# Performance work log

Measured on AMD Instinct MI355X. Metric: run time of the kernel, lower is better.

The kernel has to match this reference:

```python
import jax, jax.numpy as jnp
import numpy as np

N_NODES = 100000
N_EDGES = 1600000
N_GRAPHS = 256
IN_DIM, HID, OUT_DIM = 20, 128, 30954


def setup_inputs() -> dict:
    key = jax.random.key(0)
    ks = jax.random.split(key, 9)
    x = jax.random.normal(ks[0], (N_NODES, IN_DIM), dtype=jnp.float32)
    edge_index = jax.random.randint(ks[1], (2, N_EDGES), 0, N_NODES, dtype=jnp.int64)
    batch = jnp.sort(jax.random.randint(ks[2], (N_NODES,), 0, N_GRAPHS, dtype=jnp.int64))
    s = 0.05
    W1 = jax.random.normal(ks[3], (IN_DIM, HID), dtype=jnp.float32) * s
    b1 = jax.random.normal(ks[4], (HID,), dtype=jnp.float32) * s
    W2 = jax.random.normal(ks[5], (HID, HID), dtype=jnp.float32) * s
    b2 = jax.random.normal(ks[6], (HID,), dtype=jnp.float32) * s
    Wc = jax.random.normal(ks[7], (HID, OUT_DIM), dtype=jnp.float32) * s
    bc = jax.random.normal(ks[8], (OUT_DIM,), dtype=jnp.float32) * s
    return {"x": x, "edge_index": edge_index, "batch": batch,
            "W1": W1, "b1": b1, "W2": W2, "b2": b2, "Wc": Wc, "bc": bc}


def _gcn_norm(edge_index, n_nodes):
    # add self loops (PyG GCNConv default), symmetric normalization
    loops = jnp.arange(n_nodes, dtype=edge_index.dtype)
    src = jnp.concatenate([edge_index[0], loops])
    dst = jnp.concatenate([edge_index[1], loops])
    deg = jax.ops.segment_sum(jnp.ones_like(dst, dtype=jnp.float32), dst,
                              num_segments=n_nodes)
    dinv = jnp.where(deg > 0, jax.lax.rsqrt(deg), 0.0)
    norm = dinv[src] * dinv[dst]  # [E+N]
    return src, dst, norm


def _gcn_conv(x, src, dst, norm, W, b, n_nodes):
    h = x @ W                              # [N, out] transform first (fewer msg flops)
    msg = h[src] * norm[:, None]           # gather + scale
    out = jax.ops.segment_sum(msg, dst, num_segments=n_nodes)
    return out + b


def reference(x, edge_index, batch, W1, b1, W2, b2, Wc, bc):
    n = x.shape[0]
    src, dst, norm = _gcn_norm(edge_index, n)
    h = jax.nn.relu(_gcn_conv(x, src, dst, norm, W1, b1, n))
    # dropout is identity in eval mode
    h = jax.nn.relu(_gcn_conv(h, src, dst, norm, W2, b2, n))
    # global mean pool per graph
    sums = jax.ops.segment_sum(h, batch, num_segments=N_GRAPHS)       # [G, HID]
    cnts = jax.ops.segment_sum(jnp.ones((n,), jnp.float32), batch,
                               num_segments=N_GRAPHS)
    pooled = sums / jnp.maximum(cnts, 1.0)[:, None]
    return pooled @ Wc + bc  # [G, OUT_DIM]
```

## Files before the change

kernel.cpp:

```cpp
#include <hip/hip_runtime.h>

#define HID 128
#define SCAN_B 256

__device__ __forceinline__ float bf_lo(unsigned int u) { return __uint_as_float(u << 16); }
__device__ __forceinline__ float bf_hi(unsigned int u) { return __uint_as_float(u & 0xFFFF0000u); }
__device__ __forceinline__ unsigned short f2bf(float f) {
    unsigned int u = __float_as_uint(f);
    unsigned int r = (u + 0x7FFFu + ((u >> 16) & 1u)) >> 16;
    return (unsigned short)r;
}

__global__ void init_kernel(const unsigned int* __restrict__ p, int* __restrict__ flag,
                            float4* __restrict__ deg4, long long n4) {
    if (blockIdx.x == 0 && threadIdx.x == 0) {
        int is64 = 1;
        for (int i = 0; i < 64; ++i) {
            if (p[2 * i + 1] != 0u) { is64 = 0; break; }
        }
        *flag = is64;
    }
    long long i = (long long)blockIdx.x * blockDim.x + threadIdx.x;
    long long stride = (long long)gridDim.x * blockDim.x;
    for (; i < n4; i += stride) deg4[i] = make_float4(0.f, 0.f, 0.f, 0.f);
}

__global__ void cvtdeg_kernel(const void* __restrict__ p, int* __restrict__ out,
                              int* __restrict__ deg, int E, const int* __restrict__ flag) {
    int i = blockIdx.x * blockDim.x + threadIdx.x;
    if (i < 2 * E) {
        int v = (*flag) ? (int)((const long long*)p)[i] : ((const int*)p)[i];
        out[i] = v;
        if (i >= E) atomicAdd(&deg[v], 1);
    }
}

__global__ void cvtx_kernel(const float* __restrict__ x, unsigned short* __restrict__ xb, int n) {
    int i = blockIdx.x * blockDim.x + threadIdx.x;
    if (i < n) xb[i] = f2bf(x[i]);
}

__global__ __launch_bounds__(SCAN_B) void scan1_kernel(const int* __restrict__ deg,
                                                       int* __restrict__ incl,
                                                       int* __restrict__ blockSums, int N) {
    __shared__ int s[SCAN_B];
    int i = blockIdx.x * SCAN_B + threadIdx.x;
    int v = (i < N) ? deg[i] : 0;
    s[threadIdx.x] = v;
    __syncthreads();
#pragma unroll
    for (int off = 1; off < SCAN_B; off <<= 1) {
        int t = (threadIdx.x >= off) ? s[threadIdx.x - off] : 0;
        __syncthreads();
        s[threadIdx.x] += t;
        __syncthreads();
    }
    if (i < N) incl[i] = s[threadIdx.x];
    if (threadIdx.x == SCAN_B - 1) blockSums[blockIdx.x] = s[SCAN_B - 1];
}

__global__ __launch_bounds__(1024) void scan2_kernel(int* __restrict__ blockSums, int nb) {
    __shared__ int s[1024];
    int v = (threadIdx.x < nb) ? blockSums[threadIdx.x] : 0;
    s[threadIdx.x] = v;
    __syncthreads();
#pragma unroll
    for (int off = 1; off < 1024; off <<= 1) {
        int t = (threadIdx.x >= off) ? s[threadIdx.x - off] : 0;
        __syncthreads();
        s[threadIdx.x] += t;
        __syncthreads();
    }
    if (threadIdx.x < nb) blockSums[threadIdx.x] = (threadIdx.x > 0) ? s[threadIdx.x - 1] : 0;
}

__global__ void scan3_kernel(const int* __restrict__ incl, const int* __restrict__ deg,
                             const int* __restrict__ blockSums, int* __restrict__ rowstart,
                             float* __restrict__ dinv, int* __restrict__ cursor,
                             const void* __restrict__ bt, const int* __restrict__ flag,
                             int* __restrict__ gstart, int G,
                             int N, int E) {
    int i = blockIdx.x * blockDim.x + threadIdx.x;
    if (i < N) {
        int d = deg[i];
        rowstart[i] = incl[i] - d + blockSums[i / SCAN_B];
        dinv[i] = rsqrtf((float)(d + 1));
        cursor[i] = 0;
    }
    if (i == 0) rowstart[N] = E;
    if (i <= G) {
        int is64 = *flag;
        int lo = 0, hi = N;
        while (lo < hi) {
            int mid = (lo + hi) >> 1;
            int v = is64 ? (int)((const long long*)bt)[mid] : ((const int*)bt)[mid];
            if (v < i) lo = mid + 1; else hi = mid;
        }
        gstart[i] = lo;
    }
}

__global__ void scatter_kernel(const int* __restrict__ src, const int* __restrict__ dst,
                               const int* __restrict__ rowstart, int* __restrict__ cursor,
                               int2* __restrict__ elist, const float* __restrict__ dinv, int E) {
    int e = blockIdx.x * blockDim.x + threadIdx.x;
    if (e >= E) return;
    int s = src[e], d = dst[e];
    int pos = rowstart[d] + atomicAdd(&cursor[d], 1);
    float nm = dinv[s] * dinv[d];
    elist[pos] = make_int2(s, __float_as_int(nm));
}

__global__ __launch_bounds__(256) void agg_lin1_kernel(const float* __restrict__ x,
                                                       const unsigned int* __restrict__ xb32,
                                                       const float* __restrict__ W,
                                                       const float* __restrict__ b,
                                                       unsigned int* __restrict__ h1b,
                                                       const int* __restrict__ rowstart,
                                                       const int2* __restrict__ elist,
                                                       const float* __restrict__ dinv,
                                                       int N, int IN) {
    __shared__ float Ws[20 * HID];
    __shared__ float zs[8][20];
    const int tid = threadIdx.x;
    for (int i = tid; i < IN * HID; i += 256) Ws[i] = W[i];

    const int g      = tid >> 5;
    const int lane32 = tid & 31;
    const int slot   = lane32 >> 4;
    const int l      = lane32 & 15;
    const int node   = blockIdx.x * 8 + g;
    const int half   = IN >> 1;
    const bool act   = (node < N) && (l < half);

    float accx = 0.f, accy = 0.f;
    if (node < N) {
        int beg = rowstart[node], end = rowstart[node + 1];
        int e = beg + slot;
        for (; e + 6 < end; e += 8) {
            int2 p0 = elist[e];
            int2 p1 = elist[e + 2];
            int2 p2 = elist[e + 4];
            int2 p3 = elist[e + 6];
            unsigned int u0 = act ? xb32[(size_t)p0.x * half + l] : 0u;
            unsigned int u1 = act ? xb32[(size_t)p1.x * half + l] : 0u;
            unsigned int u2 = act ? xb32[(size_t)p2.x * half + l] : 0u;
            unsigned int u3 = act ? xb32[(size_t)p3.x * half + l] : 0u;
            float n0 = __int_as_float(p0.y), n1 = __int_as_float(p1.y);
            float n2 = __int_as_float(p2.y), n3 = __int_as_float(p3.y);
            accx += bf_lo(u0) * n0 + bf_lo(u1) * n1 + bf_lo(u2) * n2 + bf_lo(u3) * n3;
            accy += bf_hi(u0) * n0 + bf_hi(u1) * n1 + bf_hi(u2) * n2 + bf_hi(u3) * n3;
        }
        for (; e < end; e += 2) {
            int2 p0 = elist[e];
            unsigned int u0 = act ? xb32[(size_t)p0.x * half + l] : 0u;
            float n0 = __int_as_float(p0.y);
            accx += bf_lo(u0) * n0;
            accy += bf_hi(u0) * n0;
        }
    }
    accx += __shfl_xor(accx, 16, 64);
    accy += __shfl_xor(accy, 16, 64);
    if (node < N && slot == 0 && l < half) {
        float di = dinv[node];
        float dd = di * di;
        zs[g][2 * l]     = accx + x[(size_t)node * IN + 2 * l] * dd;
        zs[g][2 * l + 1] = accy + x[(size_t)node * IN + 2 * l + 1] * dd;
    }
    __syncthreads();

    if (node < N) {
        const int j = lane32;
        float4 acc4 = ((const float4*)b)[j];
        for (int k = 0; k < IN; ++k) {
            float zv = zs[g][k];
            float4 w = *(const float4*)&Ws[k * HID + j * 4];
            acc4.x += zv * w.x; acc4.y += zv * w.y;
            acc4.z += zv * w.z; acc4.w += zv * w.w;
        }
        acc4.x = fmaxf(acc4.x, 0.f); acc4.y = fmaxf(acc4.y, 0.f);
        acc4.z = fmaxf(acc4.z, 0.f); acc4.w = fmaxf(acc4.w, 0.f);
        uint2 st;
        st.x = (unsigned)f2bf(acc4.x) | ((unsigned)f2bf(acc4.y) << 16);
        st.y = (unsigned)f2bf(acc4.z) | ((unsigned)f2bf(acc4.w) << 16);
        ((uint2*)h1b)[(size_t)node * 32 + j] = st;
    }
}

#define TBM 64
#define TBN 64
#define TBK 32
#define XLD (TBM + 4)

__global__ __launch_bounds__(256) void gemm128_kernel(const unsigned int* __restrict__ Ab,
                                                      const float* __restrict__ W,
                                                      unsigned short* __restrict__ Cb, int N) {
    __shared__ float xs[TBK][XLD];
    __shared__ float wsh[TBK][TBN + 4];
    const int tid = threadIdx.x;
    const int n0 = blockIdx.x * TBM;
    const int c0 = blockIdx.y * TBN;
    const int ng = tid >> 4;
    const int cg = tid & 15;
    const int anode = tid >> 2;
    const int af    = tid & 3;
    const int wk    = tid >> 4;
    const int wc    = tid & 15;

    const uint4* Av = (const uint4*)Ab;

    float acc[4][4] = {};

    for (int k0 = 0; k0 < HID; k0 += TBK) {
        {
            int gn = n0 + anode;
            uint4 u = make_uint4(0u, 0u, 0u, 0u);
            if (gn < N) u = Av[(size_t)gn * 16 + (k0 >> 3) + af];
            int kb = af * 8;
            xs[kb + 0][anode] = bf_lo(u.x);
            xs[kb + 1][anode] = bf_hi(u.x);
            xs[kb + 2][anode] = bf_lo(u.y);
            xs[kb + 3][anode] = bf_hi(u.y);
            xs[kb + 4][anode] = bf_lo(u.z);
            xs[kb + 5][anode] = bf_hi(u.z);
            xs[kb + 6][anode] = bf_lo(u.w);
            xs[kb + 7][anode] = bf_hi(u.w);
        }
#pragma unroll
        for (int r = 0; r < 2; ++r) {
            int kk = wk + r * 16;
            *(float4*)&wsh[kk][wc * 4] =
                *(const float4*)(W + (size_t)(k0 + kk) * HID + c0 + wc * 4);
        }
        __syncthreads();
#pragma unroll
        for (int kk = 0; kk < TBK; ++kk) {
            float a[4], b[4];
            *(float4*)a = *(const float4*)&xs[kk][ng * 4];
            *(float4*)b = *(const float4*)&wsh[kk][cg * 4];
#pragma unroll
            for (int m = 0; m < 4; ++m)
#pragma unroll
                for (int n = 0; n < 4; ++n) acc[m][n] += a[m] * b[n];
        }
        __syncthreads();
    }

#pragma unroll
    for (int m = 0; m < 4; ++m) {
        int gn = n0 + ng * 4 + m;
        if (gn < N) {
            ushort4 st;
            st.x = f2bf(acc[m][0]); st.y = f2bf(acc[m][1]);
            st.z = f2bf(acc[m][2]); st.w = f2bf(acc[m][3]);
            *(ushort4*)(Cb + (size_t)gn * HID + c0 + cg * 4) = st;
        }
    }
}

__global__ __launch_bounds__(256) void csr_aggb_kernel(const unsigned short* __restrict__ h2b,
                                                       unsigned short* __restrict__ outb,
                                                       const int* __restrict__ rowstart,
                                                       const int2* __restrict__ elist,
                                                       const float* __restrict__ dinv,
                                                       const float* __restrict__ bias,
                                                       int N) {
    int node = blockIdx.x * 16 + (threadIdx.x >> 4);
    if (node >= N) return;
    int q = threadIdx.x & 15;
    const uint4* hv = (const uint4*)h2b;
    float acc[8] = {};
    int beg = rowstart[node], end = rowstart[node + 1];
    int e = beg;
    for (; e + 3 < end; e += 4) {
        int2 p0 = elist[e];
        int2 p1 = elist[e + 1];
        int2 p2 = elist[e + 2];
        int2 p3 = elist[e + 3];
        uint4 a0 = hv[(size_t)p0.x * 16 + q];
        uint4 a1 = hv[(size_t)p1.x * 16 + q];
        uint4 a2 = hv[(size_t)p2.x * 16 + q];
        uint4 a3 = hv[(size_t)p3.x * 16 + q];
        float n0 = __int_as_float(p0.y), n1 = __int_as_float(p1.y);
        float n2 = __int_as_float(p2.y), n3 = __int_as_float(p3.y);
        acc[0] += bf_lo(a0.x) * n0 + bf_lo(a1.x) * n1 + bf_lo(a2.x) * n2 + bf_lo(a3.x) * n3;
        acc[1] += bf_hi(a0.x) * n0 + bf_hi(a1.x) * n1 + bf_hi(a2.x) * n2 + bf_hi(a3.x) * n3;
        acc[2] += bf_lo(a0.y) * n0 + bf_lo(a1.y) * n1 + bf_lo(a2.y) * n2 + bf_lo(a3.y) * n3;
        acc[3] += bf_hi(a0.y) * n0 + bf_hi(a1.y) * n1 + bf_hi(a2.y) * n2 + bf_hi(a3.y) * n3;
        acc[4] += bf_lo(a0.z) * n0 + bf_lo(a1.z) * n1 + bf_lo(a2.z) * n2 + bf_lo(a3.z) * n3;
        acc[5] += bf_hi(a0.z) * n0 + bf_hi(a1.z) * n1 + bf_hi(a2.z) * n2 + bf_hi(a3.z) * n3;
        acc[6] += bf_lo(a0.w) * n0 + bf_lo(a1.w) * n1 + bf_lo(a2.w) * n2 + bf_lo(a3.w) * n3;
        acc[7] += bf_hi(a0.w) * n0 + bf_hi(a1.w) * n1 + bf_hi(a2.w) * n2 + bf_hi(a3.w) * n3;
    }
    for (; e < end; ++e) {
        int2 p0 = elist[e];
        uint4 a0 = hv[(size_t)p0.x * 16 + q];
        float n0 = __int_as_float(p0.y);
        acc[0] += bf_lo(a0.x) * n0; acc[1] += bf_hi(a0.x) * n0;
        acc[2] += bf_lo(a0.y) * n0; acc[3] += bf_hi(a0.y) * n0;
        acc[4] += bf_lo(a0.z) * n0; acc[5] += bf_hi(a0.z) * n0;
        acc[6] += bf_lo(a0.w) * n0; acc[7] += bf_hi(a0.w) * n0;
    }
    float di = dinv[node];
    float dd = di * di;
    uint4 sv = hv[(size_t)node * 16 + q];
    float self[8] = { bf_lo(sv.x), bf_hi(sv.x), bf_lo(sv.y), bf_hi(sv.y),
                      bf_lo(sv.z), bf_hi(sv.z), bf_lo(sv.w), bf_hi(sv.w) };
    float4 b0 = ((const float4*)bias)[2 * q];
    float4 b1 = ((const float4*)bias)[2 * q + 1];
    float r[8];
    r[0] = fmaxf(acc[0] + self[0] * dd + b0.x, 0.f);
    r[1] = fmaxf(acc[1] + self[1] * dd + b0.y, 0.f);
    r[2] = fmaxf(acc[2] + self[2] * dd + b0.z, 0.f);
    r[3] = fmaxf(acc[3] + self[3] * dd + b0.w, 0.f);
    r[4] = fmaxf(acc[4] + self[4] * dd + b1.x, 0.f);
    r[5] = fmaxf(acc[5] + self[5] * dd + b1.y, 0.f);
    r[6] = fmaxf(acc[6] + self[6] * dd + b1.z, 0.f);
    r[7] = fmaxf(acc[7] + self[7] * dd + b1.w, 0.f);
    uint4 st;
    st.x = (unsigned)f2bf(r[0]) | ((unsigned)f2bf(r[1]) << 16);
    st.y = (unsigned)f2bf(r[2]) | ((unsigned)f2bf(r[3]) << 16);
    st.z = (unsigned)f2bf(r[4]) | ((unsigned)f2bf(r[5]) << 16);
    st.w = (unsigned)f2bf(r[6]) | ((unsigned)f2bf(r[7]) << 16);
    ((uint4*)outb)[(size_t)node * 16 + q] = st;
}

__global__ __launch_bounds__(1024) void pool2_kernel(const unsigned short* __restrict__ hb,
                                                     const int* __restrict__ gstart,
                                                     float* __restrict__ meanp, int G) {
    int g = blockIdx.x;
    int part = threadIdx.x >> 7;
    int j = threadIdx.x & 127;
    int beg = gstart[g], end = gstart[g + 1];
    float s = 0.f;
    for (int n = beg + part; n < end; n += 8)
        s += __uint_as_float(((unsigned)hb[(size_t)n * HID + j]) << 16);
    __shared__ float red[8][HID];
    red[part][j] = s;
    __syncthreads();
    if (part == 0) {
        float tot = 0.f;
#pragma unroll
        for (int r = 0; r < 8; ++r) tot += red[r][j];
        float c = (float)(end - beg);
        meanp[(size_t)g * HID + j] = tot / fmaxf(c, 1.f);
    }
}

#define CBM 64
#define CBN 64
#define CBK 32

__global__ __launch_bounds__(256) void clsgemm_kernel(const float* __restrict__ A,
                                                      const float* __restrict__ Bw,
                                                      const float* __restrict__ bc,
                                                      float* __restrict__ C,
                                                      int G, int OUT) {
    __shared__ float as[CBK][CBM + 4];
    __shared__ float bs[CBK][CBN + 4];
    const int tid = threadIdx.x;
    const int g0 = blockIdx.y * CBM;
    const int c0 = blockIdx.x * CBN;
    const int mg = tid >> 4;
    const int cg = tid & 15;
    const int arow = tid >> 3;
    const int af   = tid & 7;
    const int wk   = tid >> 4;
    const int wc   = tid & 15;

    float acc[4][4] = {};

    for (int k0 = 0; k0 < HID; k0 += CBK) {
#pragma unroll
        for (int r = 0; r < 2; ++r) {
            int row = arow + r * 32;
            int g = g0 + row;
            float4 v = make_float4(0.f, 0.f, 0.f, 0.f);
            if (g < G) v = *(const float4*)(A + (size_t)g * HID + k0 + af * 4);
            as[af * 4 + 0][row] = v.x;
            as[af * 4 + 1][row] = v.y;
            as[af * 4 + 2][row] = v.z;
            as[af * 4 + 3][row] = v.w;
        }
#pragma unroll
        for (int r = 0; r < 2; ++r) {
            int kk = wk + r * 16;
            int c = c0 + wc * 4;
            const float* bp = Bw + (size_t)(k0 + kk) * OUT + c;
            float2 lo = make_float2(0.f, 0.f), hi = make_float2(0.f, 0.f);
            if (c + 3 < OUT) {
                lo = *(const float2*)bp;
                hi = *(const float2*)(bp + 2);
            } else {
                if (c + 0 < OUT) lo.x = bp[0];
                if (c + 1 < OUT) lo.y = bp[1];
                if (c + 2 < OUT) hi.x = bp[2];
                if (c + 3 < OUT) hi.y = bp[3];
            }
            bs[kk][wc * 4 + 0] = lo.x;
            bs[kk][wc * 4 + 1] = lo.y;
            bs[kk][wc * 4 + 2] = hi.x;
            bs[kk][wc * 4 + 3] = hi.y;
        }
        __syncthreads();
#pragma unroll
        for (int kk = 0; kk < CBK; ++kk) {
            float a[4], b[4];
            *(float4*)a = *(const float4*)&as[kk][mg * 4];
            *(float4*)b = *(const float4*)&bs[kk][cg * 4];
#pragma unroll
            for (int m = 0; m < 4; ++m)
#pragma unroll
                for (int n = 0; n < 4; ++n) acc[m][n] += a[m] * b[n];
        }
        __syncthreads();
    }

    int c = c0 + cg * 4;
    float b0 = (c + 0 < OUT) ? bc[c + 0] : 0.f;
    float b1 = (c + 1 < OUT) ? bc[c + 1] : 0.f;
    float b2 = (c + 2 < OUT) ? bc[c + 2] : 0.f;
    float b3 = (c + 3 < OUT) ? bc[c + 3] : 0.f;
#pragma unroll
    for (int m = 0; m < 4; ++m) {
        int g = g0 + mg * 4 + m;
        if (g >= G) continue;
        float* cp = C + (size_t)g * OUT + c;
        if (c + 3 < OUT) {
            *(float2*)cp = make_float2(acc[m][0] + b0, acc[m][1] + b1);
            *(float2*)(cp + 2) = make_float2(acc[m][2] + b2, acc[m][3] + b3);
        } else {
            if (c + 0 < OUT) cp[0] = acc[m][0] + b0;
            if (c + 1 < OUT) cp[1] = acc[m][1] + b1;
            if (c + 2 < OUT) cp[2] = acc[m][2] + b2;
            if (c + 3 < OUT) cp[3] = acc[m][3] + b3;
        }
    }
}

extern "C" void kernel_launch(void* const* d_in, const int* in_sizes, int n_in,
                              void* d_out, int out_size, void* d_ws, size_t ws_size,
                              hipStream_t stream) {
    const float* x  = (const float*)d_in[0];
    const void*  ei = d_in[1];
    const void*  bt = d_in[2];
    const float* W1 = (const float*)d_in[3];
    const float* b1 = (const float*)d_in[4];
    const float* W2 = (const float*)d_in[5];
    const float* b2 = (const float*)d_in[6];
    const float* Wc = (const float*)d_in[7];
    const float* bc = (const float*)d_in[8];
    float* out = (float*)d_out;

    const int N   = in_sizes[2];
    const int E   = in_sizes[1] / 2;
    const int IN  = in_sizes[0] / N;
    const int OUT = in_sizes[8];
    const int G   = out_size / OUT;

    char* ws = (char*)d_ws;
    size_t off = 0;
    auto alloc = [&](size_t bytes) {
        size_t p = off;
        off += (bytes + 255) & ~(size_t)255;
        return p;
    };
    int*            idx32    = (int*)(ws + alloc((size_t)2 * E * 4));
    int*            deg      = (int*)(ws + alloc((size_t)N * 4));
    float*          dinv     = (float*)(ws + alloc((size_t)N * 4));
    int*            incl     = (int*)(ws + alloc((size_t)N * 4));
    int*            rowstart = (int*)(ws + alloc((size_t)(N + 1) * 4));
    int*            cursor   = (int*)(ws + alloc((size_t)N * 4));
    int*            blockSums= (int*)(ws + alloc((size_t)1024 * 4));
    int2*           elist    = (int2*)(ws + alloc((size_t)E * 8));
    unsigned short* xb       = (unsigned short*)(ws + alloc((size_t)N * IN * 2));
    unsigned int*   h1b      = (unsigned int*)(ws + alloc((size_t)N * HID * 2));
    unsigned short* h2b      = (unsigned short*)(ws + alloc((size_t)N * HID * 2));
    unsigned short* houtb    = (unsigned short*)(ws + alloc((size_t)N * HID * 2));
    int*            gstart   = (int*)(ws + alloc((size_t)(G + 1) * 4));
    float*          meanp    = (float*)(ws + alloc((size_t)G * HID * 4));
    int*            flag     = (int*)(ws + alloc(4));
    (void)ws_size;

    int* srcI = idx32;
    int* dstI = idx32 + E;

    const int B = 256;
    const int nb = (N + SCAN_B - 1) / SCAN_B;

    init_kernel<<<256, B, 0, stream>>>((const unsigned int*)ei, flag, (float4*)deg,
                                       (long long)N / 4);
    cvtdeg_kernel<<<(2 * E + B - 1) / B, B, 0, stream>>>(ei, idx32, deg, E, flag);
    cvtx_kernel<<<(N * IN + B - 1) / B, B, 0, stream>>>(x, xb, N * IN);

    scan1_kernel<<<nb, SCAN_B, 0, stream>>>(deg, incl, blockSums, N);
    scan2_kernel<<<1, 1024, 0, stream>>>(blockSums, nb);
    scan3_kernel<<<(N + B - 1) / B, B, 0, stream>>>(incl, deg, blockSums, rowstart,
                                                    dinv, cursor, bt, flag, gstart, G, N, E);
    scatter_kernel<<<(E + B - 1) / B, B, 0, stream>>>(srcI, dstI, rowstart, cursor, elist, dinv, E);

    agg_lin1_kernel<<<(N + 7) / 8, 256, 0, stream>>>(x, (const unsigned int*)xb, W1, b1,
                                                     h1b, rowstart, elist, dinv, N, IN);

    {
        dim3 grid((N + TBM - 1) / TBM, HID / TBN);
        gemm128_kernel<<<grid, 256, 0, stream>>>(h1b, W2, h2b, N);
    }
    csr_aggb_kernel<<<(N + 15) / 16, 256, 0, stream>>>(h2b, houtb, rowstart, elist, dinv, b2, N);

    pool2_kernel<<<G, 1024, 0, stream>>>(houtb, gstart, meanp, G);

    {
        dim3 grid((OUT + CBN - 1) / CBN, (G + CBM - 1) / CBM);
        clsgemm_kernel<<<grid, 256, 0, stream>>>(meanp, Wc, bc, out, G, OUT);
    }
}
```

Measured before the change: 373.4 us.

## Factor symmetric GCN normalization into per-node scaling, shrink edge list to indices

Splits the edge weight dinv[s]*dinv[d] into a source-side scale, applied once per node when x is converted to bf16 and in the layer-2 GEMM epilogue, and a destination-side scale applied after aggregation. The edge list now stores only source indices (4 bytes instead of 8), which halves edge-list traffic in both aggregation passes and removes per-edge multiplies and the dinv gathers in scatter. The x conversion now runs after dinv is computed, and rounding to bf16 happens after pre-scaling, which slightly changes numerics.

Result: slower. 391.3 us (+4.8%).

```diff
diff --git a/kernel.cpp b/kernel.cpp
--- a/kernel.cpp
+++ b/kernel.cpp
@@ -35,9 +35,13 @@
     }
 }
 
-__global__ void cvtx_kernel(const float* __restrict__ x, unsigned short* __restrict__ xb, int n) {
+__global__ void cvtx_kernel(const float* __restrict__ x, const float* __restrict__ dinv,
+                            unsigned short* __restrict__ xb, int n, int IN) {
     int i = blockIdx.x * blockDim.x + threadIdx.x;
-    if (i < n) xb[i] = f2bf(x[i]);
+    if (i < n) {
+        int node = i / IN;
+        xb[i] = f2bf(x[i] * dinv[node]);
+    }
 }
 
 __global__ __launch_bounds__(SCAN_B) void scan1_kernel(const int* __restrict__ deg,
@@ -102,22 +106,20 @@
 
 __global__ void scatter_kernel(const int* __restrict__ src, const int* __restrict__ dst,
                                const int* __restrict__ rowstart, int* __restrict__ cursor,
-                               int2* __restrict__ elist, const float* __restrict__ dinv, int E) {
+                               int* __restrict__ elist, int E) {
     int e = blockIdx.x * blockDim.x + threadIdx.x;
     if (e >= E) return;
     int s = src[e], d = dst[e];
     int pos = rowstart[d] + atomicAdd(&cursor[d], 1);
-    float nm = dinv[s] * dinv[d];
-    elist[pos] = make_int2(s, __float_as_int(nm));
-}
-
-__global__ __launch_bounds__(256) void agg_lin1_kernel(const float* __restrict__ x,
-                                                       const unsigned int* __restrict__ xb32,
+    elist[pos] = s;
+}
+
+__global__ __launch_bounds__(256) void agg_lin1_kernel(const unsigned int* __restrict__ xb32,
                                                        const float* __restrict__ W,
                                                        const float* __restrict__ b,
                                                        unsigned int* __restrict__ h1b,
                                                        const int* __restrict__ rowstart,
-                                                       const int2* __restrict__ elist,
+                                                       const int* __restrict__ elist,
                                                        const float* __restrict__ dinv,
                                                        int N, int IN) {
     __shared__ float Ws[20 * HID];
@@ -138,34 +140,31 @@
         int beg = rowstart[node], end = rowstart[node + 1];
         int e = beg + slot;
         for (; e + 6 < end; e += 8) {
-            int2 p0 = elist[e];
-            int2 p1 = elist[e + 2];
-            int2 p2 = elist[e + 4];
-            int2 p3 = elist[e + 6];
-            unsigned int u0 = act ? xb32[(size_t)p0.x * half + l] : 0u;
-            unsigned int u1 = act ? xb32[(size_t)p1.x * half + l] : 0u;
-            unsigned int u2 = act ? xb32[(size_t)p2.x * half + l] : 0u;
-            unsigned int u3 = act ? xb32[(size_t)p3.x * half + l] : 0u;
-            float n0 = __int_as_float(p0.y), n1 = __int_as_float(p1.y);
-            float n2 = __int_as_float(p2.y), n3 = __int_as_float(p3.y);
-            accx += bf_lo(u0) * n0 + bf_lo(u1) * n1 + bf_lo(u2) * n2 + bf_lo(u3) * n3;
-            accy += bf_hi(u0) * n0 + bf_hi(u1) * n1 + bf_hi(u2) * n2 + bf_hi(u3) * n3;
+            int s0 = elist[e];
+            int s1 = elist[e + 2];
+            int s2 = elist[e + 4];
+            int s3 = elist[e + 6];
+            unsigned int u0 = act ? xb32[(size_t)s0 * half + l] : 0u;
+            unsigned int u1 = act ? xb32[(size_t)s1 * half + l] : 0u;
+            unsigned int u2 = act ? xb32[(size_t)s2 * half + l] : 0u;
+            unsigned int u3 = act ? xb32[(size_t)s3 * half + l] : 0u;
+            accx += bf_lo(u0) + bf_lo(u1) + bf_lo(u2) + bf_lo(u3);
+            accy += bf_hi(u0) + bf_hi(u1) + bf_hi(u2) + bf_hi(u3);
         }
         for (; e < end; e += 2) {
-            int2 p0 = elist[e];
-            unsigned int u0 = act ? xb32[(size_t)p0.x * half + l] : 0u;
-            float n0 = __int_as_float(p0.y);
-            accx += bf_lo(u0) * n0;
-            accy += bf_hi(u0) * n0;
+            int s0 = elist[e];
+            unsigned int u0 = act ? xb32[(size_t)s0 * half + l] : 0u;
+            accx += bf_lo(u0);
+            accy += bf_hi(u0);
         }
     }
     accx += __shfl_xor(accx, 16, 64);
     accy += __shfl_xor(accy, 16, 64);
     if (node < N && slot == 0 && l < half) {
         float di = dinv[node];
-        float dd = di * di;
-        zs[g][2 * l]     = accx + x[(size_t)node * IN + 2 * l] * dd;
-        zs[g][2 * l + 1] = accy + x[(size_t)node * IN + 2 * l + 1] * dd;
+        unsigned int us = xb32[(size_t)node * half + l];
+        zs[g][2 * l]     = di * (accx + bf_lo(us));
+        zs[g][2 * l + 1] = di * (accy + bf_hi(us));
     }
     __syncthreads();
 
@@ -194,6 +193,7 @@
 
 __global__ __launch_bounds__(256) void gemm128_kernel(const unsigned int* __restrict__ Ab,
                                                       const float* __restrict__ W,
+                                                      const float* __restrict__ dinv,
                                                       unsigned short* __restrict__ Cb, int N) {
     __shared__ float xs[TBK][XLD];
     __shared__ float wsh[TBK][TBN + 4];
@@ -250,9 +250,10 @@
     for (int m = 0; m < 4; ++m) {
         int gn = n0 + ng * 4 + m;
         if (gn < N) {
+            float di = dinv[gn];
             ushort4 st;
-            st.x = f2bf(acc[m][0]); st.y = f2bf(acc[m][1]);
-            st.z = f2bf(acc[m][2]); st.w = f2bf(acc[m][3]);
+            st.x = f2bf(acc[m][0] * di); st.y = f2bf(acc[m][1] * di);
+            st.z = f2bf(acc[m][2] * di); st.w = f2bf(acc[m][3] * di);
             *(ushort4*)(Cb + (size_t)gn * HID + c0 + cg * 4) = st;
         }
     }
@@ -261,7 +262,7 @@
 __global__ __launch_bounds__(256) void csr_aggb_kernel(const unsigned short* __restrict__ h2b,
                                                        unsigned short* __restrict__ outb,
                                                        const int* __restrict__ rowstart,
-                                                       const int2* __restrict__ elist,
+                                                       const int* __restrict__ elist,
                                                        const float* __restrict__ dinv,
                                                        const float* __restrict__ bias,
                                                        int N) {
@@ -273,50 +274,46 @@
     int beg = rowstart[node], end = rowstart[node + 1];
     int e = beg;
     for (; e + 3 < end; e += 4) {
-        int2 p0 = elist[e];
-        int2 p1 = elist[e + 1];
-        int2 p2 = elist[e + 2];
-        int2 p3 = elist[e + 3];
-        uint4 a0 = hv[(size_t)p0.x * 16 + q];
-        uint4 a1 = hv[(size_t)p1.x * 16 + q];
-        uint4 a2 = hv[(size_t)p2.x * 16 + q];
-        uint4 a3 = hv[(size_t)p3.x * 16 + q];
-        float n0 = __int_as_float(p0.y), n1 = __int_as_float(p1.y);
-        float n2 = __int_as_float(p2.y), n3 = __int_as_float(p3.y);
-        acc[0] += bf_lo(a0.x) * n0 + bf_lo(a1.x) * n1 + bf_lo(a2.x) * n2 + bf_lo(a3.x) * n3;
-        acc[1] += bf_hi(a0.x) * n0 + bf_hi(a1.x) * n1 + bf_hi(a2.x) * n2 + bf_hi(a3.x) * n3;
-        acc[2] += bf_lo(a0.y) * n0 + bf_lo(a1.y) * n1 + bf_lo(a2.y) * n2 + bf_lo(a3.y) * n3;
-        acc[3] += bf_hi(a0.y) * n0 + bf_hi(a1.y) * n1 + bf_hi(a2.y) * n2 + bf_hi(a3.y) * n3;
-        acc[4] += bf_lo(a0.z) * n0 + bf_lo(a1.z) * n1 + bf_lo(a2.z) * n2 + bf_lo(a3.z) * n3;
-        acc[5] += bf_hi(a0.z) * n0 + bf_hi(a1.z) * n1 + bf_hi(a2.z) * n2 + bf_hi(a3.z) * n3;
-        acc[6] += bf_lo(a0.w) * n0 + bf_lo(a1.w) * n1 + bf_lo(a2.w) * n2 + bf_lo(a3.w) * n3;
-        acc[7] += bf_hi(a0.w) * n0 + bf_hi(a1.w) * n1 + bf_hi(a2.w) * n2 + bf_hi(a3.w) * n3;
+        int s0 = elist[e];
+        int s1 = elist[e + 1];
+        int s2 = elist[e + 2];
+        int s3 = elist[e + 3];
+        uint4 a0 = hv[(size_t)s0 * 16 + q];
+        uint4 a1 = hv[(size_t)s1 * 16 + q];
+        uint4 a2 = hv[(size_t)s2 * 16 + q];
+        uint4 a3 = hv[(size_t)s3 * 16 + q];
+        acc[0] += bf_lo(a0.x) + bf_lo(a1.x) + bf_lo(a2.x) + bf_lo(a3.x);
+        acc[1] += bf_hi(a0.x) + bf_hi(a1.x) + bf_hi(a2.x) + bf_hi(a3.x);
+        acc[2] += bf_lo(a0.y) + bf_lo(a1.y) + bf_lo(a2.y) + bf_lo(a3.y);
+        acc[3] += bf_hi(a0.y) + bf_hi(a1.y) + bf_hi(a2.y) + bf_hi(a3.y);
+        acc[4] += bf_lo(a0.z) + bf_lo(a1.z) + bf_lo(a2.z) + bf_lo(a3.z);
+        acc[5] += bf_hi(a0.z) + bf_hi(a1.z) + bf_hi(a2.z) + bf_hi(a3.z);
+        acc[6] += bf_lo(a0.w) + bf_lo(a1.w) + bf_lo(a2.w) + bf_lo(a3.w);
+        acc[7] += bf_hi(a0.w) + bf_hi(a1.w) + bf_hi(a2.w) + bf_hi(a3.w);
     }
     for (; e < end; ++e) {
-        int2 p0 = elist[e];
-        uint4 a0 = hv[(size_t)p0.x * 16 + q];
-        float n0 = __int_as_float(p0.y);
-        acc[0] += bf_lo(a0.x) * n0; acc[1] += bf_hi(a0.x) * n0;
-        acc[2] += bf_lo(a0.y) * n0; acc[3] += bf_hi(a0.y) * n0;
-        acc[4] += bf_lo(a0.z) * n0; acc[5] += bf_hi(a0.z) * n0;
-        acc[6] += bf_lo(a0.w) * n0; acc[7] += bf_hi(a0.w) * n0;
+        int s0 = elist[e];
+        uint4 a0 = hv[(size_t)s0 * 16 + q];
+        acc[0] += bf_lo(a0.x); acc[1] += bf_hi(a0.x);
+        acc[2] += bf_lo(a0.y); acc[3] += bf_hi(a0.y);
+        acc[4] += bf_lo(a0.z); acc[5] += bf_hi(a0.z);
+        acc[6] += bf_lo(a0.w); acc[7] += bf_hi(a0.w);
     }
     float di = dinv[node];
-    float dd = di * di;
     uint4 sv = hv[(size_t)node * 16 + q];
     float self[8] = { bf_lo(sv.x), bf_hi(sv.x), bf_lo(sv.y), bf_hi(sv.y),
                       bf_lo(sv.z), bf_hi(sv.z), bf_lo(sv.w), bf_hi(sv.w) };
     float4 b0 = ((const float4*)bias)[2 * q];
     float4 b1 = ((const float4*)bias)[2 * q + 1];
     float r[8];
-    r[0] = fmaxf(acc[0] + self[0] * dd + b0.x, 0.f);
-    r[1] = fmaxf(acc[1] + self[1] * dd + b0.y, 0.f);
-    r[2] = fmaxf(acc[2] + self[2] * dd + b0.z, 0.f);
-    r[3] = fmaxf(acc[3] + self[3] * dd + b0.w, 0.f);
-    r[4] = fmaxf(acc[4] + self[4] * dd + b1.x, 0.f);
-    r[5] = fmaxf(acc[5] + self[5] * dd + b1.y, 0.f);
-    r[6] = fmaxf(acc[6] + self[6] * dd + b1.z, 0.f);
-    r[7] = fmaxf(acc[7] + self[7] * dd + b1.w, 0.f);
+    r[0] = fmaxf(di * (acc[0] + self[0]) + b0.x, 0.f);
+    r[1] = fmaxf(di * (acc[1] + self[1]) + b0.y, 0.f);
+    r[2] = fmaxf(di * (acc[2] + self[2]) + b0.z, 0.f);
+    r[3] = fmaxf(di * (acc[3] + self[3]) + b0.w, 0.f);
+    r[4] = fmaxf(di * (acc[4] + self[4]) + b1.x, 0.f);
+    r[5] = fmaxf(di * (acc[5] + self[5]) + b1.y, 0.f);
+    r[6] = fmaxf(di * (acc[6] + self[6]) + b1.z, 0.f);
+    r[7] = fmaxf(di * (acc[7] + self[7]) + b1.w, 0.f);
     uint4 st;
     st.x = (unsigned)f2bf(r[0]) | ((unsigned)f2bf(r[1]) << 16);
     st.y = (unsigned)f2bf(r[2]) | ((unsigned)f2bf(r[3]) << 16);
@@ -472,7 +469,7 @@
     int*            rowstart = (int*)(ws + alloc((size_t)(N + 1) * 4));
     int*            cursor   = (int*)(ws + alloc((size_t)N * 4));
     int*            blockSums= (int*)(ws + alloc((size_t)1024 * 4));
-    int2*           elist    = (int2*)(ws + alloc((size_t)E * 8));
+    int*            elist    = (int*)(ws + alloc((size_t)E * 4));
     unsigned short* xb       = (unsigned short*)(ws + alloc((size_t)N * IN * 2));
     unsigned int*   h1b      = (unsigned int*)(ws + alloc((size_t)N * HID * 2));
     unsigned short* h2b      = (unsigned short*)(ws + alloc((size_t)N * HID * 2));
@@ -491,20 +488,20 @@
     init_kernel<<<256, B, 0, stream>>>((const unsigned int*)ei, flag, (float4*)deg,
                                        (long long)N / 4);
     cvtdeg_kernel<<<(2 * E + B - 1) / B, B, 0, stream>>>(ei, idx32, deg, E, flag);
-    cvtx_kernel<<<(N * IN + B - 1) / B, B, 0, stream>>>(x, xb, N * IN);
 
     scan1_kernel<<<nb, SCAN_B, 0, stream>>>(deg, incl, blockSums, N);
     scan2_kernel<<<1, 1024, 0, stream>>>(blockSums, nb);
     scan3_kernel<<<(N + B - 1) / B, B, 0, stream>>>(incl, deg, blockSums, rowstart,
                                                     dinv, cursor, bt, flag, gstart, G, N, E);
-    scatter_kernel<<<(E + B - 1) / B, B, 0, stream>>>(srcI, dstI, rowstart, cursor, elist, dinv, E);
-
-    agg_lin1_kernel<<<(N + 7) / 8, 256, 0, stream>>>(x, (const unsigned int*)xb, W1, b1,
+    cvtx_kernel<<<(N * IN + B - 1) / B, B, 0, stream>>>(x, dinv, xb, N * IN, IN);
+    scatter_kernel<<<(E + B - 1) / B, B, 0, stream>>>(srcI, dstI, rowstart, cursor, elist, E);
+
+    agg_lin1_kernel<<<(N + 7) / 8, 256, 0, stream>>>((const unsigned int*)xb, W1, b1,
                                                      h1b, rowstart, elist, dinv, N, IN);
 
     {
         dim3 grid((N + TBM - 1) / TBM, HID / TBN);
-        gemm128_kernel<<<grid, 256, 0, stream>>>(h1b, W2, h2b, N);
+        gemm128_kernel<<<grid, 256, 0, stream>>>(h1b, W2, dinv, h2b, N);
     }
     csr_aggb_kernel<<<(N + 15) / 16, 256, 0, stream>>>(h2b, houtb, rowstart, elist, dinv, b2, N);
 
```
